# Optimization experiments

Hardware: AMD Instinct MI355X
Metric: run time of the kernel (lower is better)

The kernel has to match this reference:

```python
import jax, jax.numpy as jnp
import numpy as np

B, C, O, A, H, W, K = 4, 256, 256, 9, 96, 96, 3
ROOT = 3            # isqrt(num_experts)
HID = 2 * A         # gate hidden dim
EPS = 1e-5          # InstanceNorm / BatchNorm eps


def _silu(x):
    return x * jax.nn.sigmoid(x)


def setup_inputs() -> dict:
    key = jax.random.key(0)
    ks = jax.random.split(key, 8)
    s = lambda k, shape, sc: jax.random.normal(k, shape, jnp.float32) * sc
    return {
        "x": jax.random.normal(ks[0], (B, C, H, W), jnp.float32),
        "w_expert": s(ks[1], (C * A, 1, K, K), 0.1),   # depthwise conv, torch OIHW with I=1
        "w_g1": s(ks[2], (HID, A), 0.3),
        "b_g1": s(ks[3], (HID,), 0.1),
        "w_g2": s(ks[4], (A, HID), 0.3),
        "b_g2": s(ks[5], (A,), 0.1),
        "w_proj": s(ks[6], (O, C), 0.05),               # 1x1 conv weight
        "bn_gamma": jnp.ones((O,), jnp.float32),
        "bn_beta": jnp.zeros((O,), jnp.float32),
    }


def reference(x, w_expert, w_g1, b_g1, w_g2, b_g2, w_proj, bn_gamma, bn_beta):
    # ---- Gate: AdaptiveAvgPool2d((3,3)) -> MLP -> sigmoid -------------------
    # H,W divisible by ROOT so adaptive pool == exact block mean
    pooled = x.reshape(B, C, ROOT, H // ROOT, ROOT, W // ROOT).mean(axis=(3, 5))  # [B,C,3,3]
    g = pooled.reshape(B, C, A)
    g = _silu(g @ w_g1.T + b_g1)
    weights = jax.nn.sigmoid(g @ w_g2.T + b_g2)  # [B,C,A]

    # ---- depthwise expert conv: groups=C, out=C*A ---------------------------
    y = jax.lax.conv_general_dilated(
        x, w_expert, window_strides=(1, 1), padding=[(1, 1), (1, 1)],
        dimension_numbers=("NCHW", "OIHW", "NCHW"), feature_group_count=C,
    )  # [B, C*A, H, W]; channels [c*A:(c+1)*A] come from input channel c

    # ---- InstanceNorm2d (no affine) + SiLU ----------------------------------
    mu = y.mean(axis=(2, 3), keepdims=True)
    var = y.var(axis=(2, 3), keepdims=True)  # biased, matches torch InstanceNorm
    y = _silu((y - mu) * jax.lax.rsqrt(var + EPS))

    # ---- gated weighted sum over expert dim ---------------------------------
    y = y.reshape(B, C, A, H, W)
    moe = jnp.einsum("bcahw,bca->bchw", y, weights)

    # ---- out_project: 1x1 conv (no bias) + BatchNorm2d (batch stats) + SiLU --
    z = jnp.einsum("bchw,oc->bohw", moe, w_proj)
    bm = z.mean(axis=(0, 2, 3), keepdims=True)
    bv = z.var(axis=(0, 2, 3), keepdims=True)  # biased var used for normalization
    z = (z - bm) * jax.lax.rsqrt(bv + EPS)
    z = z * bn_gamma[None, :, None, None] + bn_beta[None, :, None, None]
    return _silu(z)
```

## Files before the change

kernel.cpp:

```cpp
#include <hip/hip_runtime.h>
#include <math.h>

#define BB 4
#define CC 256
#define OO 256
#define HH 96
#define WW 96
#define HW (HH*WW)
#define HIDN 18
#define EPS 1e-5f
#define TS 100

__device__ __forceinline__ float sigmoidf_(float x) {
    return __builtin_amdgcn_rcpf(1.0f + __expf(-x));
}
__device__ __forceinline__ float siluf_(float x) { return x * sigmoidf_(x); }

__global__ __launch_bounds__(256)
void k_wt(const float* __restrict__ w, float* __restrict__ wt)
{
    const int c = blockIdx.x, o = threadIdx.x;
    wt[c * OO + o] = w[o * CC + c];
}

__global__ __launch_bounds__(256)
void k_moe(const float* __restrict__ x,
           const float* __restrict__ w_expert,
           const float* __restrict__ w_g1, const float* __restrict__ b_g1,
           const float* __restrict__ w_g2, const float* __restrict__ b_g2,
           float* __restrict__ moe)
{
    __shared__ float tile[98 * TS];
    __shared__ float wexp[81];
    __shared__ float pool[9];
    __shared__ float hbuf[HIDN];
    __shared__ float wgt[9];
    __shared__ float stat[18];
    __shared__ float mu_s[9], rstd_s[9];

    const int bc  = blockIdx.x;
    const int c   = bc & (CC - 1);
    const int tid = threadIdx.x;

    if (tid < 98) { tile[tid] = 0.0f; tile[97 * TS + tid] = 0.0f; }
    if (tid < 96) { tile[(tid + 1) * TS] = 0.0f; tile[(tid + 1) * TS + 97] = 0.0f; }
    if (tid < 18) stat[tid] = 0.0f;
    if (tid < 9)  pool[tid] = 0.0f;
    if (tid < 81) wexp[tid] = w_expert[c * 81 + tid];
    __syncthreads();

    const float4* xp4 = (const float4*)(x + (size_t)bc * HW);
    for (int idx = tid; idx < HW / 4; idx += 256) {
        int r = idx / 24, q = idx - r * 24;
        float4 v = xp4[idx];
        float* t = &tile[(r + 1) * TS + q * 4 + 1];
        t[0] = v.x; t[1] = v.y; t[2] = v.z; t[3] = v.w;
    }
    __syncthreads();

    for (int r = 0; r < 9; ++r) {
        const int i0 = (r / 3) * 32, j0 = (r % 3) * 32;
        float s = 0.0f;
        for (int idx = tid; idx < 1024; idx += 256) {
            int rr = idx >> 5, cc2 = idx & 31;
            s += tile[(i0 + rr + 1) * TS + (j0 + cc2 + 1)];
        }
        #pragma unroll
        for (int off = 1; off < 64; off <<= 1) s += __shfl_xor(s, off, 64);
        if ((tid & 63) == 0) atomicAdd(&pool[r], s);
    }
    __syncthreads();

    if (tid < HIDN) {
        float acc = b_g1[tid];
        #pragma unroll
        for (int j = 0; j < 9; ++j)
            acc += (pool[j] * (1.0f / 1024.0f)) * w_g1[tid * 9 + j];
        hbuf[tid] = siluf_(acc);
    }
    __syncthreads();
    if (tid < 9) {
        float acc = b_g2[tid];
        #pragma unroll
        for (int k = 0; k < HIDN; ++k) acc += hbuf[k] * w_g2[tid * HIDN + k];
        wgt[tid] = sigmoidf_(acc);
    }
    __syncthreads();

    float wre[81];
    #pragma unroll
    for (int i = 0; i < 81; ++i) wre[i] = wexp[i];

    float sum[9], sq[9];
    #pragma unroll
    for (int a = 0; a < 9; ++a) { sum[a] = 0.0f; sq[a] = 0.0f; }

    for (int qi = tid; qi < HW / 4; qi += 256) {
        int r  = qi / 24;
        int c4 = (qi - r * 24) << 2;
        const float* t0 = &tile[r * TS + c4];
        float4 a0 = *(const float4*)t0;        float2 e0 = *(const float2*)(t0 + 4);
        float4 a1 = *(const float4*)(t0 + TS); float2 e1 = *(const float2*)(t0 + TS + 4);
        float4 a2 = *(const float4*)(t0 + 2*TS); float2 e2 = *(const float2*)(t0 + 2*TS + 4);
        float w0[6] = {a0.x, a0.y, a0.z, a0.w, e0.x, e0.y};
        float w1[6] = {a1.x, a1.y, a1.z, a1.w, e1.x, e1.y};
        float w2[6] = {a2.x, a2.y, a2.z, a2.w, e2.x, e2.y};
        #pragma unroll
        for (int a = 0; a < 9; ++a) {
            const float k0 = wre[a*9+0], k1 = wre[a*9+1], k2 = wre[a*9+2];
            const float k3 = wre[a*9+3], k4 = wre[a*9+4], k5 = wre[a*9+5];
            const float k6 = wre[a*9+6], k7 = wre[a*9+7], k8 = wre[a*9+8];
            #pragma unroll
            for (int j = 0; j < 4; ++j) {
                float v = w0[j] * k0;
                v = fmaf(w0[j+1], k1, v); v = fmaf(w0[j+2], k2, v);
                v = fmaf(w1[j],   k3, v); v = fmaf(w1[j+1], k4, v);
                v = fmaf(w1[j+2], k5, v); v = fmaf(w2[j],   k6, v);
                v = fmaf(w2[j+1], k7, v); v = fmaf(w2[j+2], k8, v);
                sum[a] += v;
                sq[a]   = fmaf(v, v, sq[a]);
            }
        }
    }
    #pragma unroll
    for (int a = 0; a < 9; ++a) {
        float s = sum[a], q = sq[a];
        #pragma unroll
        for (int off = 1; off < 64; off <<= 1) {
            s += __shfl_xor(s, off, 64);
            q += __shfl_xor(q, off, 64);
        }
        if ((tid & 63) == 0) { atomicAdd(&stat[a], s); atomicAdd(&stat[9 + a], q); }
    }
    __syncthreads();
    if (tid < 9) {
        float m = stat[tid] * (1.0f / HW);
        float v = stat[9 + tid] * (1.0f / HW) - m * m;
        mu_s[tid]   = m;
        rstd_s[tid] = rsqrtf(v + EPS);
    }
    __syncthreads();

    float ms_r[9], rs_r[9], wg_r[9];
    #pragma unroll
    for (int a = 0; a < 9; ++a) {
        rs_r[a] = rstd_s[a];
        ms_r[a] = mu_s[a] * rs_r[a];
        wg_r[a] = wgt[a];
    }

    float* mpn = moe + (size_t)bc * HW;
    for (int qi = tid; qi < HW / 4; qi += 256) {
        int r  = qi / 24;
        int c4 = (qi - r * 24) << 2;
        const float* t0 = &tile[r * TS + c4];
        float4 a0 = *(const float4*)t0;        float2 e0 = *(const float2*)(t0 + 4);
        float4 a1 = *(const float4*)(t0 + TS); float2 e1 = *(const float2*)(t0 + TS + 4);
        float4 a2 = *(const float4*)(t0 + 2*TS); float2 e2 = *(const float2*)(t0 + 2*TS + 4);
        float w0[6] = {a0.x, a0.y, a0.z, a0.w, e0.x, e0.y};
        float w1[6] = {a1.x, a1.y, a1.z, a1.w, e1.x, e1.y};
        float w2[6] = {a2.x, a2.y, a2.z, a2.w, e2.x, e2.y};
        float oq[4] = {0.f, 0.f, 0.f, 0.f};
        #pragma unroll
        for (int a = 0; a < 9; ++a) {
            const float k0 = wre[a*9+0], k1 = wre[a*9+1], k2 = wre[a*9+2];
            const float k3 = wre[a*9+3], k4 = wre[a*9+4], k5 = wre[a*9+5];
            const float k6 = wre[a*9+6], k7 = wre[a*9+7], k8 = wre[a*9+8];
            #pragma unroll
            for (int j = 0; j < 4; ++j) {
                float v = w0[j] * k0;
                v = fmaf(w0[j+1], k1, v); v = fmaf(w0[j+2], k2, v);
                v = fmaf(w1[j],   k3, v); v = fmaf(w1[j+1], k4, v);
                v = fmaf(w1[j+2], k5, v); v = fmaf(w2[j],   k6, v);
                v = fmaf(w2[j+1], k7, v); v = fmaf(w2[j+2], k8, v);
                float t = fmaf(v, rs_r[a], -ms_r[a]);
                oq[j] = fmaf(wg_r[a], t * sigmoidf_(t), oq[j]);
            }
        }
        *(float4*)(mpn + r * 96 + c4) = make_float4(oq[0], oq[1], oq[2], oq[3]);
    }
}

#define GOT 16
#define GPT 512

#define FMA4(A, S, M) { A.x = fmaf(S, M.x, A.x); A.y = fmaf(S, M.y, A.y); \
                        A.z = fmaf(S, M.z, A.z); A.w = fmaf(S, M.w, A.w); }

__global__ __launch_bounds__(256)
void k_gemm(const float* __restrict__ moe, const float* __restrict__ wt,
            float* __restrict__ z, float* __restrict__ stats)
{
    const int tid  = threadIdx.x;
    const int wv   = tid >> 6;
    const int lane = tid & 63;
    const int wo   = wv & 1;
    const int wp   = wv >> 1;
    const int b    = blockIdx.z;

    const int obase = blockIdx.y * GOT + wo * 8;
    const int obu   = __builtin_amdgcn_readfirstlane(obase);
    const int pbase = blockIdx.x * GPT + wp * 256 + lane * 4;

    const float* mptr = moe + (size_t)b * CC * HW + pbase;

    float4 acc[8];
    #pragma unroll
    for (int i = 0; i < 8; ++i) acc[i] = make_float4(0.f, 0.f, 0.f, 0.f);

    #pragma unroll 1
    for (int c = 0; c < CC; c += 4) {
        float4 mv[4];
        #pragma unroll
        for (int u = 0; u < 4; ++u)
            mv[u] = *(const float4*)(mptr + (size_t)(c + u) * HW);
        #pragma unroll
        for (int u = 0; u < 4; ++u) {
            const float* wr = wt + (size_t)(c + u) * OO + obu;
            float4 wa = *(const float4*)wr;
            float4 wb = *(const float4*)(wr + 4);
            FMA4(acc[0], wa.x, mv[u]); FMA4(acc[1], wa.y, mv[u]);
            FMA4(acc[2], wa.z, mv[u]); FMA4(acc[3], wa.w, mv[u]);
            FMA4(acc[4], wb.x, mv[u]); FMA4(acc[5], wb.y, mv[u]);
            FMA4(acc[6], wb.z, mv[u]); FMA4(acc[7], wb.w, mv[u]);
        }
    }

    #pragma unroll
    for (int oi = 0; oi < 8; ++oi) {
        *(float4*)(z + ((size_t)b * OO + obase + oi) * HW + pbase) = acc[oi];
        float s = acc[oi].x + acc[oi].y + acc[oi].z + acc[oi].w;
        float q = fmaf(acc[oi].x, acc[oi].x, fmaf(acc[oi].y, acc[oi].y,
                  fmaf(acc[oi].z, acc[oi].z, acc[oi].w * acc[oi].w)));
        #pragma unroll
        for (int off = 1; off < 64; off <<= 1) {
            s += __shfl_xor(s, off, 64);
            q += __shfl_xor(q, off, 64);
        }
        if (lane == 0) {
            atomicAdd(&stats[obu + oi], s);
            atomicAdd(&stats[OO + obu + oi], q);
        }
    }
}

__global__ __launch_bounds__(256)
void k_bnsilu(const float* __restrict__ z, const float* __restrict__ stats,
              const float* __restrict__ gamma, const float* __restrict__ beta,
              float* __restrict__ out)
{
    const int o = blockIdx.y;
    const int b = blockIdx.z;
    const float invn = 1.0f / (float)(BB * HW);
    const float m  = stats[o] * invn;
    const float vv = fmaf(-m, m, stats[OO + o] * invn);
    const float rs = rsqrtf(vv + EPS);
    const float g  = gamma[o] * rs;
    const float bb = fmaf(-m, g, beta[o]);

    const size_t base = ((size_t)b * OO + o) * HW;
    const int i = (blockIdx.x * 256 + threadIdx.x) * 4;
    float4 v = *(const float4*)(z + base + i);
    v.x = siluf_(fmaf(v.x, g, bb));
    v.y = siluf_(fmaf(v.y, g, bb));
    v.z = siluf_(fmaf(v.z, g, bb));
    v.w = siluf_(fmaf(v.w, g, bb));
    *(float4*)(out + base + i) = v;
}

extern "C" void kernel_launch(void* const* d_in, const int* in_sizes, int n_in,
                              void* d_out, int out_size, void* d_ws, size_t ws_size,
                              hipStream_t stream)
{
    const float* x        = (const float*)d_in[0];
    const float* w_expert = (const float*)d_in[1];
    const float* w_g1     = (const float*)d_in[2];
    const float* b_g1     = (const float*)d_in[3];
    const float* w_g2     = (const float*)d_in[4];
    const float* b_g2     = (const float*)d_in[5];
    const float* w_proj   = (const float*)d_in[6];
    const float* bn_g     = (const float*)d_in[7];
    const float* bn_b     = (const float*)d_in[8];
    float* out = (float*)d_out;

    float* z     = (float*)d_ws;
    float* stats = z + (size_t)BB * OO * HW;
    float* wt    = stats + 2 * OO;
    float* moe   = out;

    hipMemsetAsync(stats, 0, 2 * OO * sizeof(float), stream);

    k_wt<<<CC, 256, 0, stream>>>(w_proj, wt);
    k_moe<<<BB * CC, 256, 0, stream>>>(x, w_expert, w_g1, b_g1, w_g2, b_g2, moe);
    k_gemm<<<dim3(HW / GPT, OO / GOT, BB), 256, 0, stream>>>(moe, wt, z, stats);
    k_bnsilu<<<dim3(HW / 4 / 256, OO, BB), 256, 0, stream>>>(z, stats, bn_g, bn_b, out);
}
```

Measured before the change: 332.3 us.

## Remap GEMM blocks for XCD locality, load expert weights directly, coarsen BN-SiLU

The expert conv weights are now read straight from global memory through a uniform pointer (likely scalar loads) instead of being staged in LDS and copied into registers. The GEMM launch becomes a 1D grid with a swizzled block-to-tile mapping so that blocks landing on the same XCD share output-channel tiles and pixel tiles, which is meant to improve L2 reuse of the moe activations. The BN+SiLU kernel now processes a whole channel plane per block with a 9-step unrolled loop, cutting block count. The risk is that repeated global weight loads inside the hot loops add latency if the compiler does not hoist them into scalar registers.

```diff
diff --git a/kernel.cpp b/kernel.cpp
--- a/kernel.cpp
+++ b/kernel.cpp
@@ -31,7 +31,6 @@
            float* __restrict__ moe)
 {
     __shared__ float tile[98 * TS];
-    __shared__ float wexp[81];
     __shared__ float pool[9];
     __shared__ float hbuf[HIDN];
     __shared__ float wgt[9];
@@ -41,12 +40,12 @@
     const int bc  = blockIdx.x;
     const int c   = bc & (CC - 1);
     const int tid = threadIdx.x;
+    const float* __restrict__ we = w_expert + c * 81;
 
     if (tid < 98) { tile[tid] = 0.0f; tile[97 * TS + tid] = 0.0f; }
     if (tid < 96) { tile[(tid + 1) * TS] = 0.0f; tile[(tid + 1) * TS + 97] = 0.0f; }
     if (tid < 18) stat[tid] = 0.0f;
     if (tid < 9)  pool[tid] = 0.0f;
-    if (tid < 81) wexp[tid] = w_expert[c * 81 + tid];
     __syncthreads();
 
     const float4* xp4 = (const float4*)(x + (size_t)bc * HW);
@@ -86,10 +85,6 @@
         wgt[tid] = sigmoidf_(acc);
     }
     __syncthreads();
-
-    float wre[81];
-    #pragma unroll
-    for (int i = 0; i < 81; ++i) wre[i] = wexp[i];
 
     float sum[9], sq[9];
     #pragma unroll
@@ -107,9 +102,9 @@
         float w2[6] = {a2.x, a2.y, a2.z, a2.w, e2.x, e2.y};
         #pragma unroll
         for (int a = 0; a < 9; ++a) {
-            const float k0 = wre[a*9+0], k1 = wre[a*9+1], k2 = wre[a*9+2];
-            const float k3 = wre[a*9+3], k4 = wre[a*9+4], k5 = wre[a*9+5];
-            const float k6 = wre[a*9+6], k7 = wre[a*9+7], k8 = wre[a*9+8];
+            const float k0 = we[a*9+0], k1 = we[a*9+1], k2 = we[a*9+2];
+            const float k3 = we[a*9+3], k4 = we[a*9+4], k5 = we[a*9+5];
+            const float k6 = we[a*9+6], k7 = we[a*9+7], k8 = we[a*9+8];
             #pragma unroll
             for (int j = 0; j < 4; ++j) {
                 float v = w0[j] * k0;
@@ -163,9 +158,9 @@
         float oq[4] = {0.f, 0.f, 0.f, 0.f};
         #pragma unroll
         for (int a = 0; a < 9; ++a) {
-            const float k0 = wre[a*9+0], k1 = wre[a*9+1], k2 = wre[a*9+2];
-            const float k3 = wre[a*9+3], k4 = wre[a*9+4], k5 = wre[a*9+5];
-            const float k6 = wre[a*9+6], k7 = wre[a*9+7], k8 = wre[a*9+8];
+            const float k0 = we[a*9+0], k1 = we[a*9+1], k2 = we[a*9+2];
+            const float k3 = we[a*9+3], k4 = we[a*9+4], k5 = we[a*9+5];
+            const float k6 = we[a*9+6], k7 = we[a*9+7], k8 = we[a*9+8];
             #pragma unroll
             for (int j = 0; j < 4; ++j) {
                 float v = w0[j] * k0;
@@ -191,16 +186,23 @@
 void k_gemm(const float* __restrict__ moe, const float* __restrict__ wt,
             float* __restrict__ z, float* __restrict__ stats)
 {
+    const int id   = blockIdx.x;
+    const int cls  = id & 7;
+    const int m    = id >> 3;
+    const int ot   = m & 15;
+    const int g    = (m >> 4) * 8 + cls;
+    const int b    = g / 18;
+    const int pt   = g - b * 18;
+
     const int tid  = threadIdx.x;
     const int wv   = tid >> 6;
     const int lane = tid & 63;
     const int wo   = wv & 1;
     const int wp   = wv >> 1;
-    const int b    = blockIdx.z;
-
-    const int obase = blockIdx.y * GOT + wo * 8;
+
+    const int obase = ot * GOT + wo * 8;
     const int obu   = __builtin_amdgcn_readfirstlane(obase);
-    const int pbase = blockIdx.x * GPT + wp * 256 + lane * 4;
+    const int pbase = pt * GPT + wp * 256 + lane * 4;
 
     const float* mptr = moe + (size_t)b * CC * HW + pbase;
 
@@ -258,14 +260,18 @@
     const float g  = gamma[o] * rs;
     const float bb = fmaf(-m, g, beta[o]);
 
-    const size_t base = ((size_t)b * OO + o) * HW;
-    const int i = (blockIdx.x * 256 + threadIdx.x) * 4;
-    float4 v = *(const float4*)(z + base + i);
-    v.x = siluf_(fmaf(v.x, g, bb));
-    v.y = siluf_(fmaf(v.y, g, bb));
-    v.z = siluf_(fmaf(v.z, g, bb));
-    v.w = siluf_(fmaf(v.w, g, bb));
-    *(float4*)(out + base + i) = v;
+    const float4* zp = (const float4*)(z + ((size_t)b * OO + o) * HW);
+    float4*       op = (float4*)(out + ((size_t)b * OO + o) * HW);
+    #pragma unroll
+    for (int j = 0; j < 9; ++j) {
+        const int i = j * 256 + threadIdx.x;
+        float4 v = zp[i];
+        v.x = siluf_(fmaf(v.x, g, bb));
+        v.y = siluf_(fmaf(v.y, g, bb));
+        v.z = siluf_(fmaf(v.z, g, bb));
+        v.w = siluf_(fmaf(v.w, g, bb));
+        op[i] = v;
+    }
 }
 
 extern "C" void kernel_launch(void* const* d_in, const int* in_sizes, int n_in,
@@ -292,6 +298,6 @@
 
     k_wt<<<CC, 256, 0, stream>>>(w_proj, wt);
     k_moe<<<BB * CC, 256, 0, stream>>>(x, w_expert, w_g1, b_g1, w_g2, b_g2, moe);
-    k_gemm<<<dim3(HW / GPT, OO / GOT, BB), 256, 0, stream>>>(moe, wt, z, stats);
-    k_bnsilu<<<dim3(HW / 4 / 256, OO, BB), 256, 0, stream>>>(z, stats, bn_g, bn_b, out);
-}
+    k_gemm<<<BB * (HW / GPT) * (OO / GOT), 256, 0, stream>>>(moe, wt, z, stats);
+    k_bnsilu<<<dim3(1, OO, BB), 256, 0, stream>>>(z, stats, bn_g, bn_b, out);
+}
```

Measured after the change: 286.4 us. -13.8%, faster.
